# Kernel tuning notes

Measured on AMD Instinct MI355X. Metric: run time of the kernel, lower is better.

The kernel has to match this reference:

```python
import jax, jax.numpy as jnp
import numpy as np

W_PRIOR_STD = 1.0          # w_prior_stddev
OBS_STD = 1.0              # observational_noise_stddev
EPS = 1e-7                 # keras backend.epsilon()
B, E, K, C = 64, 32, 128, 512


def setup_inputs() -> dict:
    key = jax.random.key(0)
    k1, k2, k3, k4 = jax.random.split(key, 4)
    x = jax.random.normal(k1, (B, E, C), jnp.float32)
    prior_memory_mean = jax.random.normal(k2, (K, C), jnp.float32)  # truncated_normal(0,1) init
    prior_log_variance_scale = jax.random.uniform(k3, (), jnp.float32)  # scalar weight (init zeros; nonzero for testing)
    log_w_stddev = jnp.float32(0.3)  # constant(initial_w_stddev) init
    z_noise = jax.random.normal(k4, (E, B, C), jnp.float32)  # reparam noise for z_distribution.sample()
    return {"x": x, "prior_memory_mean": prior_memory_mean,
            "prior_log_variance_scale": prior_log_variance_scale,
            "log_w_stddev": log_w_stddev, "z_noise": z_noise}


def _kl_w(w, sw, k):
    # KL( N(w, sw^2 I_k) || N(0, w_prior^2 I_k) ), w_prior = 1
    return 0.5 * (k * sw * sw + jnp.sum(w * w, axis=-1) - k - 2.0 * k * jnp.log(sw))


def reference(x, prior_memory_mean, prior_log_variance_scale, log_w_stddev, z_noise):
    b, e, c = x.shape
    k = prior_memory_mean.shape[0]
    dt = x.dtype
    sw = jnp.exp(log_w_stddev)                      # w_stddev
    lam = (OBS_STD ** 2) / (W_PRIOR_STD ** 2)       # l2 regularizer in w-solve
    I_k = jnp.eye(k, dtype=dt)

    # prior state (tiled over batch)
    M0 = jnp.broadcast_to(prior_memory_mean[None], (b, k, c)) + jnp.zeros((b, k, c), dt)
    var = prior_log_variance_scale + EPS
    U0 = jnp.broadcast_to(var * I_k, (b, k, k)) + jnp.zeros((b, k, k), dt)

    z = jnp.transpose(x, (1, 0, 2))  # [E,B,C]

    def solve_w(M, z_t):
        # least squares: w = (M M^T + lam I)^{-1} M z  -> [B,K]
        A = jnp.einsum('bkc,blc->bkl', M, M) + lam * I_k
        rhs = jnp.einsum('bkc,bc->bk', M, z_t)
        return jnp.linalg.solve(A, rhs[..., None])[..., 0]

    def step(carry, z_t):
        M, U = carry                                    # [B,K,C], [B,K,K]
        w = solve_w(M, z_t)                             # memory sample == mean; iteration_count == 1
        delta = z_t - jnp.einsum('bk,bkc->bc', w, M)    # prediction delta [B,C]
        wU = jnp.einsum('bk,bkl->bl', w, U)             # cross variance [B,K]
        sigma = jnp.sum(wU * w, axis=-1) + OBS_STD ** 2 # z episode covariance [B]
        gain = wU / sigma[:, None]                      # [B,K]
        M_new = M + gain[..., None] * delta[:, None, :] # rank-1 Kalman update
        U_new = U - jnp.einsum('bk,bl->bkl', gain, wU)
        return (M_new, U_new), _kl_w(w, sw, k)          # per-step w divergence [B]

    (M_post, U_post), kl_episode = jax.lax.scan(step, (M0, U0), z)  # kl_episode [E,B]

    # read memory: batched solve with shared Gram matrix over episode
    A = jnp.einsum('bkc,blc->bkl', M_post, M_post) + lam * I_k
    rhs = jnp.einsum('bkc,ebc->bke', M_post, z)
    w_read = jnp.transpose(jnp.linalg.solve(A, rhs), (2, 0, 1))     # [E,B,K]
    z_mean = jnp.einsum('ebk,bkc->ebc', w_read, M_post)
    kl_read = _kl_w(w_read, sw, k)                                  # [E,B]

    total_divergence = jnp.mean(kl_episode + kl_read)               # add_loss value
    z_sample = z_mean + OBS_STD * z_noise                           # reparameterized sample
    return jnp.transpose(z_sample, (1, 0, 2)), total_divergence
```

## Files before the change

### kernel.cpp

```cpp
#include <hip/hip_runtime.h>

#define BB 64
#define EE 32
#define KK 128
#define CC 512
#define V0EPS 1e-7f

#define LTR 132
#define PTS 132
#define LKM 36
#define L36 36
#define LWT 176
#define SEG(i) ((((i) >> 4) * 20) + ((i) & 15))

#define SC_S2  0
#define SC_SIG 1
#define SC_KL  2
#define SC_B1  3
#define SC_B2  4
#define SC_R11 5
#define SC_R12 6
#define SC_R22 7

__device__ __forceinline__ float wsum64(float v) {
#pragma unroll
  for (int m = 32; m >= 1; m >>= 1) v += __shfl_xor(v, m, 64);
  return v;
}

__device__ __forceinline__ float wsum32(float v) {
#pragma unroll
  for (int m = 16; m >= 1; m >>= 1) v += __shfl_xor(v, m, 64);
  return v;
}

__device__ __forceinline__ float dot4(const float4 a, const float4 b) {
  return a.x * b.x + a.y * b.y + a.z * b.z + a.w * b.w;
}

__global__ __launch_bounds__(256) void a0_kernel(const float* __restrict__ M0,
                                                 float* __restrict__ wsA0) {
  __shared__ __align__(16) float sRow[CC];
  const int k = blockIdx.x >> 1, half = blockIdx.x & 1;
  for (int c = threadIdx.x; c < CC; c += 256) sRow[c] = M0[k * CC + c];
  __syncthreads();
  const int wv = threadIdx.x >> 6, ln = threadIdx.x & 63;
  const float4* zr = (const float4*)(sRow + 8 * ln);
  const float4 z0 = zr[0], z1 = zr[1];
  for (int li = 0; li < 16; ++li) {
    const int l = half * 64 + wv * 16 + li;
    const float4* rp = (const float4*)(M0 + l * CC + 8 * ln);
    const float4 a = rp[0], b = rp[1];
    float s = dot4(a, z0) + dot4(b, z1);
    s = wsum64(s);
    if (ln == 0) wsA0[k * KK + l] = s + (l == k ? 1.0f : 0.0f);
  }
}

__global__ __launch_bounds__(1024) void psinv_kernel(const float* __restrict__ x,
                                                     const float* __restrict__ M0,
                                                     float* __restrict__ wsP,
                                                     float* __restrict__ wsSp,
                                                     const float* __restrict__ A0g,
                                                     float* __restrict__ Ainv0) {
  __shared__ __align__(16) float zAll[32][520];
  __shared__ __align__(16) float Mch[2][16][520];
  __shared__ float sFb[2][128];
  __shared__ __align__(16) float sPv[2][256];
  __shared__ float sScal[2];
  const int tid = threadIdx.x;

  if (blockIdx.x > 0) {
    const int b = (blockIdx.x - 1) >> 2, kq = (blockIdx.x - 1) & 3;
    {
      const float4* x4 = (const float4*)(x + (size_t)b * EE * CC);
#pragma unroll
      for (int i = 0; i < 4; i++) {
        const int F = tid + 1024 * i, e = F >> 7, c4 = F & 127;
        ((float4*)zAll[e])[c4] = x4[F];
      }
    }
    const float4* M4 = (const float4*)M0;
    const int srow = tid >> 7, sc4 = tid & 127;
    const int kbase = kq * 32;
    float4 st0 = M4[(kbase + srow) * 128 + sc4];
    float4 st1 = M4[(kbase + 8 + srow) * 128 + sc4];
    int buf = 0;
    const int p = tid & 7;
    const int ep = (tid >> 3) & 15;
    const int kp = tid >> 7;
#pragma unroll 1
    for (int kc = 0; kc < 2; ++kc) {
      ((float4*)Mch[buf][srow])[sc4] = st0;
      ((float4*)Mch[buf][8 + srow])[sc4] = st1;
      __syncthreads();
      if (kc == 0) {
        st0 = M4[(kbase + 16 + srow) * 128 + sc4];
        st1 = M4[(kbase + 24 + srow) * 128 + sc4];
      }
      float s00 = 0, s01 = 0, s10 = 0, s11 = 0;
      const float* m0 = Mch[buf][kp];
      const float* m1 = Mch[buf][kp + 8];
      const float* z0 = zAll[2 * ep];
      const float* z1 = zAll[2 * ep + 1];
#pragma unroll
      for (int u = 0; u < 16; u++) {
        const int c = 4 * p + 32 * u;
        const float4 a0 = *(const float4*)(m0 + c);
        const float4 a1 = *(const float4*)(m1 + c);
        const float4 b0 = *(const float4*)(z0 + c);
        const float4 b1 = *(const float4*)(z1 + c);
        s00 += dot4(a0, b0); s01 += dot4(a0, b1);
        s10 += dot4(a1, b0); s11 += dot4(a1, b1);
      }
#pragma unroll
      for (int m = 1; m <= 4; m <<= 1) {
        s00 += __shfl_xor(s00, m, 64); s01 += __shfl_xor(s01, m, 64);
        s10 += __shfl_xor(s10, m, 64); s11 += __shfl_xor(s11, m, 64);
      }
      if (p == 0) {
        float* Pb = wsP + (size_t)b * KK * EE;
        Pb[(kbase + kc * 16 + kp) * EE + 2 * ep] = s00;
        Pb[(kbase + kc * 16 + kp) * EE + 2 * ep + 1] = s01;
        Pb[(kbase + kc * 16 + kp + 8) * EE + 2 * ep] = s10;
        Pb[(kbase + kc * 16 + kp + 8) * EE + 2 * ep + 1] = s11;
      }
      buf ^= 1;
    }
    {
      const int e = tid >> 5, f = tid & 31;
      const float4* ze = ((const float4*)zAll[e]) + 32 * kq;
      const float4* zf = ((const float4*)zAll[f]) + 32 * kq;
      float a0 = 0, a1 = 0, a2 = 0, a3 = 0;
#pragma unroll 4
      for (int u = 0; u < 32; u++) {
        const float4 A = ze[u], Bq = zf[u];
        a0 += A.x * Bq.x; a1 += A.y * Bq.y; a2 += A.z * Bq.z; a3 += A.w * Bq.w;
      }
      wsSp[((size_t)b * 4 + kq) * 1024 + e * EE + f] = (a0 + a1) + (a2 + a3);
    }
  } else {
    const int r = tid >> 3, q = tid & 7;
    float wreg[16], vreg[16];
    {
      const float4* a4 = (const float4*)(A0g + r * KK + 16 * q);
#pragma unroll
      for (int u = 0; u < 4; u++) {
        const float4 t4 = a4[u];
        wreg[4 * u] = t4.x; wreg[4 * u + 1] = t4.y; wreg[4 * u + 2] = t4.z; wreg[4 * u + 3] = t4.w;
      }
#pragma unroll
      for (int c = 0; c < 16; c++) vreg[c] = (16 * q + c == r) ? 1.0f : 0.0f;
    }
    if (q == 0) sFb[0][r] = wreg[0];
    if (r == 0) {
#pragma unroll
      for (int c = 0; c < 16; c++) { sPv[0][16 * q + c] = wreg[c]; sPv[0][128 + 16 * q + c] = vreg[c]; }
    }
    if (tid == 0) sScal[0] = 1.0f / wreg[0];
    __syncthreads();
#pragma unroll 1
    for (int j = 0; j < KK; ++j) {
      const int sl = j & 1, sn = sl ^ 1;
      const float f = sFb[sl][r] * sScal[sl];
      if (r != j) {
        if (16 * q + 15 >= j) {
          const float4* w4 = (const float4*)(sPv[sl] + 16 * q);
#pragma unroll
          for (int u = 0; u < 4; u++) {
            const float4 aa = w4[u];
            wreg[4 * u] -= f * aa.x; wreg[4 * u + 1] -= f * aa.y;
            wreg[4 * u + 2] -= f * aa.z; wreg[4 * u + 3] -= f * aa.w;
          }
        }
        if (16 * q <= j) {
          const float4* v4 = (const float4*)(sPv[sl] + 128 + 16 * q);
#pragma unroll
          for (int u = 0; u < 4; u++) {
            const float4 bb = v4[u];
            vreg[4 * u] -= f * bb.x; vreg[4 * u + 1] -= f * bb.y;
            vreg[4 * u + 2] -= f * bb.z; vreg[4 * u + 3] -= f * bb.w;
          }
        }
      }
      if (j + 1 < KK) {
        const int jn = j + 1;
        float wval = 0.0f;
#pragma unroll
        for (int c = 0; c < 16; c++) if (c == (jn & 15)) wval = wreg[c];
        if (q == (jn >> 4)) sFb[sn][r] = wval;
        if (r == jn) {
#pragma unroll
          for (int c = 0; c < 16; c++) { sPv[sn][16 * q + c] = wreg[c]; sPv[sn][128 + 16 * q + c] = vreg[c]; }
        }
        if (r == jn && q == (jn >> 4)) sScal[sn] = 1.0f / wval;
      }
      __syncthreads();
    }
    {
      float dval = 0.0f;
#pragma unroll
      for (int c = 0; c < 16; c++) if (c == (r & 15)) dval = wreg[c];
      if (q == (r >> 4)) sFb[0][r] = dval;
    }
    __syncthreads();
    {
      const float sc = 1.0f / sFb[0][r];
      float4* o4 = (float4*)(Ainv0 + r * KK + 16 * q);
#pragma unroll
      for (int u = 0; u < 4; u++) {
        float4 o;
        o.x = vreg[4 * u] * sc; o.y = vreg[4 * u + 1] * sc;
        o.z = vreg[4 * u + 2] * sc; o.w = vreg[4 * u + 3] * sc;
        o4[u] = o;
      }
    }
  }
}

__global__ __launch_bounds__(1024) void scan_kernel(
    const float* __restrict__ Pg, const float* __restrict__ Sg,
    const float* __restrict__ scaleP, const float* __restrict__ Ainv0,
    float* __restrict__ wsKL, float* __restrict__ wsKLr, float* __restrict__ wsWt) {
  __shared__ __align__(16) float sPT[EE * PTS];
  __shared__ __align__(16) float sGT[EE * LTR];
  __shared__ __align__(16) float sEggT[EE * LTR];
  __shared__ __align__(16) float uni2[EE * LTR];
  __shared__ __align__(16) float uni3[KK * LKM];
  __shared__ __align__(16) float uni1[KK * LKM];
  __shared__ __align__(16) float sEk[KK * LKM];
  __shared__ __align__(16) float sS[EE * L36];
  __shared__ __align__(16) float sD[EE * L36];
  __shared__ __align__(16) float sW[160];
  __shared__ __align__(16) float sWU[160];
  __shared__ __align__(16) float sPu[160];
  __shared__ __align__(16) float sPm[160];
  __shared__ __align__(16) float sQ[160];
  __shared__ __align__(16) float sDz[EE];
  __shared__ __align__(16) float sDgw[EE];
  __shared__ __align__(16) float sQt[EE];
  __shared__ __align__(16) float sScal[16];

  float* sYT = uni2;
  float* sGk = uni3;
  float* sYk = uni1;

  const int tid = threadIdx.x, ln = tid & 63;
  const int mr = (tid >> 2) & 127, mq = tid & 3;
  const int b = blockIdx.x;

  float areg[32];
  if (tid < 512) {
    const float4* a4 = (const float4*)(Ainv0 + mr * KK + 32 * mq);
#pragma unroll
    for (int u = 0; u < 8; u++) {
      const float4 t4 = a4[u];
      areg[4 * u] = t4.x; areg[4 * u + 1] = t4.y; areg[4 * u + 2] = t4.z; areg[4 * u + 3] = t4.w;
    }
  }
  {
    const float* Pb = Pg + (size_t)b * KK * EE;
#pragma unroll
    for (int i = 0; i < 4; i++) {
      const int idx = tid + 1024 * i;
      sPT[(idx & 31) * PTS + (idx >> 5)] = Pb[idx];
    }
    const float* Sb = Sg + (size_t)b * 4096;
    sS[(tid >> 5) * L36 + (tid & 31)] =
        Sb[tid] + Sb[tid + 1024] + Sb[tid + 2048] + Sb[tid + 3072];
  }
  if (tid < 16) sScal[tid] = 0.0f;
  const float v0 = scaleP[0] + V0EPS;
  __syncthreads();
  if (tid < 512) {
    const float* xb = sPT + 32 * mq;
    float s = 0;
#pragma unroll
    for (int c = 0; c < 32; c++) s += areg[c] * xb[c];
    s += __shfl_xor(s, 1, 64); s += __shfl_xor(s, 2, 64);
    if (mq == 0) sW[SEG(mr)] = s;
  }
  __syncthreads();

#pragma unroll 1
  for (int t = 0; t < EE; ++t) {
    const bool hn = (t + 1 < EE);
    if (tid < 512) {
      const float* xb = sW + 40 * mq;
      float s = 0;
#pragma unroll
      for (int c = 0; c < 16; c++) s += areg[c] * xb[c];
#pragma unroll
      for (int c = 0; c < 16; c++) s += areg[16 + c] * xb[20 + c];
      s += __shfl_xor(s, 1, 64); s += __shfl_xor(s, 2, 64);
      if (mq == 0) sPm[SEG(mr)] = s;
    } else if (tid < 768) {
      const int s8 = (tid - 512) >> 3, p3 = tid & 7;
      if (s8 < t) {
        const float* gr = sGT + s8 * LTR + 16 * p3;
        const float* wr_ = sW + 20 * p3;
        float s = 0;
#pragma unroll
        for (int kk = 0; kk < 16; kk++) s += gr[kk] * wr_[kk];
        s += __shfl_xor(s, 1, 64); s += __shfl_xor(s, 2, 64); s += __shfl_xor(s, 4, 64);
        if (p3 == 0) sDgw[s8] = s;
      } else if (s8 == 31) {
        const float* wp = sW + 20 * p3;
        float s = 0;
#pragma unroll
        for (int kk = 0; kk < 16; kk++) s += wp[kk] * wp[kk];
        s += __shfl_xor(s, 1, 64); s += __shfl_xor(s, 2, 64); s += __shfl_xor(s, 4, 64);
        if (p3 == 0) sScal[SC_S2] = s;
      }
    } else {
      const int j = (tid - 768) >> 3, p3 = tid & 7;
      if (j < t) {
        const float* yr = sYT + j * LTR + 16 * p3;
        const float* wr_ = sW + 20 * p3;
        float s = 0;
#pragma unroll
        for (int kk = 0; kk < 16; kk++) s += yr[kk] * wr_[kk];
        s += __shfl_xor(s, 1, 64); s += __shfl_xor(s, 2, 64); s += __shfl_xor(s, 4, 64);
        if (p3 == 0) sQt[j] = s;
      }
    }
    __syncthreads();
    if (tid < 256) {
      const int k = tid >> 1, h = tid & 1;
      const float* yk = sYk + k * LKM + 16 * h;
      const float* qb = sQt + 16 * h;
      float a = 0;
#pragma unroll
      for (int u = 0; u < 16; u++) {
        const int j = 16 * h + u;
        a += (j < t) ? yk[u] * qb[u] : 0.0f;
      }
      a += __shfl_xor(a, 1, 64);
      if (h == 0) sWU[SEG(k)] = v0 * sW[SEG(k)] - a;
    } else if (tid < 384) {
      const int r2 = (tid - 256) >> 2, p = tid & 3;
      float a = 0;
#pragma unroll
      for (int u = 0; u < 8; u++) {
        const int s2 = p + 4 * u;
        a += (s2 < t) ? sDgw[s2] * sD[s2 * L36 + r2] : 0.0f;
      }
      a += __shfl_xor(a, 1, 64); a += __shfl_xor(a, 2, 64);
      if (p == 0) sD[t * L36 + r2] = ((r2 == t) ? 1.0f : 0.0f) - a;
    } else if (tid < 448) {
      float a = sW[SEG(ln)] * sPm[SEG(ln)] + sW[SEG(ln + 64)] * sPm[SEG(ln + 64)];
      a = wsum64(a);
      if (ln == 0) sScal[SC_R22] = a;
    } else if (tid < 512) {
      const float s2v = sScal[SC_S2];
      float a = (ln < t) ? sQt[ln] * sQt[ln] : 0.0f;
      a = wsum64(a);
      if (ln == 0) {
        sScal[SC_SIG] = v0 * s2v - a + 1.0f;
        sScal[SC_KL] += s2v;
      }
    } else if (tid < 640) {
      const int k = tid - 512;
      float a = sW[SEG(k)];
      const float* ek = sEk + k * LKM;
      const int nc = (t + 3) >> 2;
#pragma unroll 1
      for (int c4 = 0; c4 < nc; ++c4) {
        const float4 ev = *(const float4*)(ek + 4 * c4);
        const float4 dv = *(const float4*)(sDgw + 4 * c4);
        const int u0 = 4 * c4;
        a -= ((u0 + 0 < t) ? ev.x * dv.x : 0.0f) + ((u0 + 1 < t) ? ev.y * dv.y : 0.0f) +
             ((u0 + 2 < t) ? ev.z * dv.z : 0.0f) + ((u0 + 3 < t) ? ev.w * dv.w : 0.0f);
      }
      sEk[k * LKM + t] = a;
      sEggT[t * LTR + k] = a;
    } else if (tid < 896) {
      const int s4 = (tid - 640) >> 3, p3 = tid & 7;
      if (hn && s4 < t) {
        const float* er = sEggT + s4 * LTR + 16 * p3;
        const float* pr = sPT + (t + 1) * PTS + 16 * p3;
        float a = 0;
#pragma unroll
        for (int kk = 0; kk < 16; kk++) a -= er[kk] * pr[kk];
        const float4 dv = *(const float4*)(sD + s4 * L36 + 4 * p3);
        const float4 sv = *(const float4*)(sS + (t + 1) * L36 + 4 * p3);
        a += dot4(dv, sv);
        a += __shfl_xor(a, 1, 64); a += __shfl_xor(a, 2, 64); a += __shfl_xor(a, 4, 64);
        if (p3 == 0) sDz[s4] = a;
      }
    }
    __syncthreads();
    if (tid < 512) {
      const float* xb = sWU + 40 * mq;
      float s = 0;
#pragma unroll
      for (int c = 0; c < 16; c++) s += areg[c] * xb[c];
#pragma unroll
      for (int c = 0; c < 16; c++) s += areg[16 + c] * xb[20 + c];
      s += __shfl_xor(s, 1, 64); s += __shfl_xor(s, 2, 64);
      if (mq == 0) sPu[SEG(mr)] = s;
    } else if (tid < 576) {
      if (hn) {
        float a = -(sEggT[t * LTR + ln] * sPT[(t + 1) * PTS + ln] +
                    sEggT[t * LTR + ln + 64] * sPT[(t + 1) * PTS + ln + 64]);
        if (ln < 32) a += sD[t * L36 + ln] * sS[(t + 1) * L36 + ln];
        a = wsum64(a);
        if (ln == 0) sDz[t] = a;
      }
    } else if (tid < 640) {
      float a = sEggT[t * LTR + ln] * sPT[t * PTS + ln] +
                sEggT[t * LTR + ln + 64] * sPT[t * PTS + ln + 64];
      a = wsum64(a);
      if (ln == 0) sScal[SC_B2] = a;
    } else if (tid < 704) {
      if (ln < 32) {
        float a = sD[t * L36 + ln] * sS[t * L36 + ln];
        a = wsum32(a);
        if (ln == 0) sScal[SC_B1] = a;
      } else {
        const int k0 = (ln - 32) * 4;
        const float4 wu4 = *(const float4*)(sWU + SEG(k0));
        const float4 pm4 = *(const float4*)(sPm + SEG(k0));
        float a = dot4(wu4, pm4);
        a = wsum32(a);
        if (ln == 32) sScal[SC_R12] = a;
      }
    } else if (tid < 768) {
      const float sig = sScal[SC_SIG];
      const float rsq = rsqrtf(sig);
#pragma unroll
      for (int u = 0; u < 2; u++) {
        const int k = ln + 64 * u;
        const float wu = sWU[SEG(k)];
        const float gv = wu / sig;
        const float yv = wu * rsq;
        sGT[t * LTR + k] = gv;
        sGk[k * LKM + t] = gv;
        sYT[t * LTR + k] = yv;
        sYk[k * LKM + t] = yv;
      }
    }
    __syncthreads();
    if (tid < 512) {
      if (hn) {
        const float* gk = sGk + mr * LKM + 8 * mq;
        const float* dzb = sDz + 8 * mq;
        float a = 0;
#pragma unroll
        for (int u = 0; u < 8; u++) {
          const int s2 = 8 * mq + u;
          a += (s2 < t) ? gk[u] * dzb[u] : 0.0f;
        }
        a += __shfl_xor(a, 1, 64); a += __shfl_xor(a, 2, 64);
        if (mq == 0)
          sQ[SEG(mr)] = sPT[(t + 1) * PTS + mr] + a + (sWU[SEG(mr)] / sScal[SC_SIG]) * sDz[t];
      }
    } else if (tid < 576) {
      float a = sWU[SEG(ln)] * sPu[SEG(ln)] + sWU[SEG(ln + 64)] * sPu[SEG(ln + 64)];
      a = wsum64(a);
      if (ln == 0) sScal[SC_R11] = a;
    }
    __syncthreads();
    if (tid < 512) {
      {
        const float4 sc0 = *(const float4*)(sScal);
        const float4 sc1 = *(const float4*)(sScal + 4);
        const float rs = 1.0f / sc0.y;
        const float beta = sc0.w - sc1.x - sc0.x;
        const float e11 = sc1.y * rs * rs;
        const float e12 = sc1.z * rs + 1.0f;
        const float e22 = sc1.w - beta;
        const float rd = 1.0f / (e11 * e22 - e12 * e12);
        const float t11 = e22 * rd, t12 = -e12 * rd, t22 = e11 * rd;
        const float u1r = sPu[SEG(mr)] * rs, u2r = sPm[SEG(mr)];
        const float* pub = sPu + 40 * mq;
        const float* pmb = sPm + 40 * mq;
#pragma unroll
        for (int c = 0; c < 16; c++) {
          const float u1c = pub[c] * rs;
          const float u2c = pmb[c];
          areg[c] -= u1r * (t11 * u1c + t12 * u2c) + u2r * (t12 * u1c + t22 * u2c);
        }
#pragma unroll
        for (int c = 0; c < 16; c++) {
          const float u1c = pub[20 + c] * rs;
          const float u2c = pmb[20 + c];
          areg[16 + c] -= u1r * (t11 * u1c + t12 * u2c) + u2r * (t12 * u1c + t22 * u2c);
        }
      }
      if (hn) {
        const float* xb = sQ + 40 * mq;
        float s = 0;
#pragma unroll
        for (int c = 0; c < 16; c++) s += areg[c] * xb[c];
#pragma unroll
        for (int c = 0; c < 16; c++) s += areg[16 + c] * xb[20 + c];
        s += __shfl_xor(s, 1, 64); s += __shfl_xor(s, 2, 64);
        if (mq == 0) sW[SEG(mr)] = s;
      }
    }
    __syncthreads();
  }

  float* sR1T  = uni2;
  float* sGamT = uni2 + 1152;
  float* sRhsT = uni1;
  float* sWrT  = uni3;
  if (tid == 0) wsKL[b] = sScal[SC_KL];

  {
    const int s = tid >> 5, e = tid & 31;
    const float4* er = (const float4*)(sEggT + s * LTR);
    const float4* pr = (const float4*)(sPT + e * PTS);
    float a = 0;
#pragma unroll 8
    for (int u = 0; u < 32; ++u) a -= dot4(er[u], pr[u]);
    const float4* dr = (const float4*)(sD + s * L36);
    const float4* sr = (const float4*)(sS + e * L36);
#pragma unroll
    for (int u = 0; u < 8; ++u) a += dot4(dr[u], sr[u]);
    sR1T[e * 36 + s] = a;
  }
  __syncthreads();
  {
    const int k = tid & 127, e8 = tid >> 7;
    float4 g0, g1, g2, g3, g4, g5, g6, g7;
    {
      const float4* gk = (const float4*)(sGk + k * LKM);
      g0 = gk[0]; g1 = gk[1]; g2 = gk[2]; g3 = gk[3];
      g4 = gk[4]; g5 = gk[5]; g6 = gk[6]; g7 = gk[7];
    }
#pragma unroll
    for (int u = 0; u < 4; ++u) {
      const int e = e8 * 4 + u;
      const float4* r1 = (const float4*)(sR1T + e * 36);
      float a = sPT[e * PTS + k];
      a += dot4(g0, r1[0]) + dot4(g1, r1[1]) + dot4(g2, r1[2]) + dot4(g3, r1[3]);
      a += dot4(g4, r1[4]) + dot4(g5, r1[5]) + dot4(g6, r1[6]) + dot4(g7, r1[7]);
      sRhsT[e * PTS + k] = a;
    }
  }
  __syncthreads();
  if (tid < 512) {
#pragma unroll 2
    for (int e = 0; e < EE; ++e) {
      const float* xb = sRhsT + e * PTS + 32 * mq;
      float s = 0;
#pragma unroll
      for (int c = 0; c < 32; c++) s += areg[c] * xb[c];
      s += __shfl_xor(s, 1, 64); s += __shfl_xor(s, 2, 64);
      if (mq == 0) sWrT[e * PTS + mr] = s;
    }
  }
  __syncthreads();
  {
    const int s = tid >> 5, e = tid & 31;
    const float4* gr = (const float4*)(sGT + s * LTR);
    const float4* wr = (const float4*)(sWrT + e * PTS);
    float a = 0;
#pragma unroll 8
    for (int u = 0; u < 32; ++u) a += dot4(gr[u], wr[u]);
    sGamT[e * 36 + s] = a;
  }
  __syncthreads();
  {
    const int k = tid & 127, e8 = tid >> 7;
    float4 E0, E1, E2, E3, E4, E5, E6, E7;
    {
      const float4* ek = (const float4*)(sEk + k * LKM);
      E0 = ek[0]; E1 = ek[1]; E2 = ek[2]; E3 = ek[3];
      E4 = ek[4]; E5 = ek[5]; E6 = ek[6]; E7 = ek[7];
    }
#pragma unroll
    for (int u = 0; u < 4; ++u) {
      const int e = e8 * 4 + u;
      const float4* gm = (const float4*)(sGamT + e * 36);
      float a = sWrT[e * PTS + k];
      a -= dot4(E0, gm[0]) + dot4(E1, gm[1]) + dot4(E2, gm[2]) + dot4(E3, gm[3]);
      a -= dot4(E4, gm[4]) + dot4(E5, gm[5]) + dot4(E6, gm[6]) + dot4(E7, gm[7]);
      wsWt[(size_t)b * 5120 + e * 160 + k] = a;
    }
  }
  {
    const int e = tid & 31, sp = tid >> 5;
    float4 gm[8];
    {
      const float4* g4 = (const float4*)(sGamT + e * 36);
#pragma unroll
      for (int u = 0; u < 8; ++u) gm[u] = g4[u];
    }
    float a = 0;
#pragma unroll
    for (int u = 0; u < 8; ++u) {
      const float4 g = gm[u];
      a += sD[(4 * u + 0) * L36 + sp] * g.x + sD[(4 * u + 1) * L36 + sp] * g.y +
           sD[(4 * u + 2) * L36 + sp] * g.z + sD[(4 * u + 3) * L36 + sp] * g.w;
    }
    wsWt[(size_t)b * 5120 + e * 160 + 128 + sp] = a;
  }
  {
    const int e = tid >> 5, p = tid & 31;
    const float4 w0 = *(const float4*)(sWrT + e * PTS + 4 * p);
    float a = dot4(w0, w0);
    a = wsum32(a);
    if ((tid & 31) == 0) wsKLr[b * EE + e] = a;
  }
}

__global__ __launch_bounds__(512) void postBF_kernel(
    const float* __restrict__ wsWt, const float* __restrict__ x,
    const float* __restrict__ M0, const float* __restrict__ znoise,
    const float* __restrict__ wsKL, const float* __restrict__ wsKLr,
    const float* __restrict__ lwsP, float* __restrict__ out) {
  __shared__ __align__(16) float sWtT[32 * LWT];
  __shared__ __align__(16) float Mch[2 * 16 * 132];
  const int tid = threadIdx.x;

  if (blockIdx.x == 256) {
    float* sPp = sWtT;
    float s = 0.0f;
    if (tid < 64) s += wsKL[tid];
    for (int i = tid; i < 2048; i += 512) s += wsKLr[i];
    sPp[tid] = s;
    __syncthreads();
    for (int off = 256; off > 0; off >>= 1) {
      if (tid < off) sPp[tid] += sPp[tid + off];
      __syncthreads();
    }
    if (tid == 0) {
      const float lws = lwsP[0];
      const float sw2 = expf(2.0f * lws);
      out[(size_t)BB * EE * CC] =
          0.5f * sPp[0] / (float)(EE * BB) + (float)KK * (sw2 - 1.0f - 2.0f * lws);
    }
    return;
  }

  const int b = blockIdx.x >> 2, cq = blockIdx.x & 3;
  {
    const int e = tid >> 4, j = tid & 15;
    const float* Wg = wsWt + (size_t)b * 5120 + e * 160;
#pragma unroll
    for (int u = 0; u < 10; ++u) sWtT[e * LWT + j + 16 * u] = Wg[j + 16 * u];
  }
  const int srow = tid >> 5, sc4 = tid & 31;
  const int e = tid & 31, cs = tid >> 5;
  const float* xb = x + (size_t)b * EE * CC;
  const int cbase = cq * 128;
  float4 st = *(const float4*)(M0 + srow * CC + cbase + 4 * sc4);
  float acc[8];
#pragma unroll
  for (int u = 0; u < 8; u++) acc[u] = 0.0f;
  int buf = 0;
#pragma unroll 1
  for (int ch2 = 0; ch2 < 10; ++ch2) {
    *(float4*)(Mch + buf * 2112 + srow * 132 + 4 * sc4) = st;
    __syncthreads();
    if (ch2 + 1 < 10) {
      const int row = (ch2 + 1) * 16 + srow;
      st = (row < 128) ? *(const float4*)(M0 + row * CC + cbase + 4 * sc4)
                       : *(const float4*)(xb + (row - 128) * CC + cbase + 4 * sc4);
    }
    const float4* wt4 = (const float4*)(sWtT + e * LWT + ch2 * 16);
    const float4 wa = wt4[0], wb = wt4[1], wc = wt4[2], wd = wt4[3];
    const float wv16[16] = {wa.x, wa.y, wa.z, wa.w, wb.x, wb.y, wb.z, wb.w,
                            wc.x, wc.y, wc.z, wc.w, wd.x, wd.y, wd.z, wd.w};
#pragma unroll
    for (int kk = 0; kk < 16; ++kk) {
      const float* mrp = Mch + buf * 2112 + kk * 132 + cs * 8;
      const float4 m0 = *(const float4*)(mrp);
      const float4 m1 = *(const float4*)(mrp + 4);
      const float wk = wv16[kk];
      acc[0] += wk * m0.x; acc[1] += wk * m0.y; acc[2] += wk * m0.z; acc[3] += wk * m0.w;
      acc[4] += wk * m1.x; acc[5] += wk * m1.y; acc[6] += wk * m1.z; acc[7] += wk * m1.w;
    }
    buf ^= 1;
  }
  {
    const size_t ob = ((size_t)b * EE + e) * CC + cbase + cs * 8;
    const size_t nb = ((size_t)e * BB + b) * CC + cbase + cs * 8;
#pragma unroll
    for (int u = 0; u < 2; u++) {
      const float4 nz = *(const float4*)(znoise + nb + 4 * u);
      float4 o;
      o.x = acc[4 * u] + nz.x;     o.y = acc[4 * u + 1] + nz.y;
      o.z = acc[4 * u + 2] + nz.z; o.w = acc[4 * u + 3] + nz.w;
      *(float4*)(out + ob + 4 * u) = o;
    }
  }
}

extern "C" void kernel_launch(void* const* d_in, const int* in_sizes, int n_in,
                              void* d_out, int out_size, void* d_ws, size_t ws_size,
                              hipStream_t stream) {
  (void)in_sizes; (void)n_in; (void)out_size; (void)ws_size;
  const float* x = (const float*)d_in[0];
  const float* M0 = (const float*)d_in[1];
  const float* scaleP = (const float*)d_in[2];
  const float* lwsP = (const float*)d_in[3];
  const float* znoise = (const float*)d_in[4];
  float* out = (float*)d_out;

  float* ws = (float*)d_ws;
  float* wsP = ws;
  float* wsSp = wsP + 262144;
  float* wsA0 = wsSp + 262144;
  float* wsAinv0 = wsA0 + 16384;
  float* wsKL = wsAinv0 + 16384;
  float* wsKLr = wsKL + 64;
  float* wsWt = wsKLr + 2048;

  a0_kernel<<<256, 256, 0, stream>>>(M0, wsA0);
  psinv_kernel<<<257, 1024, 0, stream>>>(x, M0, wsP, wsSp, wsA0, wsAinv0);
  scan_kernel<<<BB, 1024, 0, stream>>>(wsP, wsSp, scaleP, wsAinv0,
                                       wsKL, wsKLr, wsWt);
  postBF_kernel<<<257, 512, 0, stream>>>(wsWt, x, M0, znoise, wsKL, wsKLr, lwsP, out);
}
```

Before: 287.9 us.

## Block Gauss-Jordan inversion two pivots per step to halve barriers

The Gauss-Jordan inverse of the initial Gram matrix in block 0 of psinv_kernel now eliminates two pivot columns per iteration using a 2x2 block pivot. This runs 64 iterations and 64 barriers instead of 128, with double-buffered shared pivot rows and columns. The cost is more shared loads and arithmetic per iteration and a slightly different rounding order. It only helps if block 0's serial inversion is on the critical path relative to the other blocks.

```diff
diff --git a/kernel.cpp b/kernel.cpp
--- a/kernel.cpp
+++ b/kernel.cpp
@@ -65,9 +65,8 @@
                                                      float* __restrict__ Ainv0) {
   __shared__ __align__(16) float zAll[32][520];
   __shared__ __align__(16) float Mch[2][16][520];
-  __shared__ float sFb[2][128];
-  __shared__ __align__(16) float sPv[2][256];
-  __shared__ float sScal[2];
+  __shared__ __align__(16) float sFb[2][2][128];
+  __shared__ __align__(16) float sPv[2][2][256];
   const int tid = threadIdx.x;
 
   if (blockIdx.x > 0) {
@@ -152,48 +151,72 @@
 #pragma unroll
       for (int c = 0; c < 16; c++) vreg[c] = (16 * q + c == r) ? 1.0f : 0.0f;
     }
-    if (q == 0) sFb[0][r] = wreg[0];
+    if (q == 0) { sFb[0][0][r] = wreg[0]; sFb[0][1][r] = wreg[1]; }
     if (r == 0) {
 #pragma unroll
-      for (int c = 0; c < 16; c++) { sPv[0][16 * q + c] = wreg[c]; sPv[0][128 + 16 * q + c] = vreg[c]; }
-    }
-    if (tid == 0) sScal[0] = 1.0f / wreg[0];
+      for (int c = 0; c < 16; c++) { sPv[0][0][16 * q + c] = wreg[c]; sPv[0][0][128 + 16 * q + c] = vreg[c]; }
+    }
+    if (r == 1) {
+#pragma unroll
+      for (int c = 0; c < 16; c++) { sPv[0][1][16 * q + c] = wreg[c]; sPv[0][1][128 + 16 * q + c] = vreg[c]; }
+    }
     __syncthreads();
 #pragma unroll 1
-    for (int j = 0; j < KK; ++j) {
-      const int sl = j & 1, sn = sl ^ 1;
-      const float f = sFb[sl][r] * sScal[sl];
-      if (r != j) {
-        if (16 * q + 15 >= j) {
-          const float4* w4 = (const float4*)(sPv[sl] + 16 * q);
-#pragma unroll
-          for (int u = 0; u < 4; u++) {
-            const float4 aa = w4[u];
-            wreg[4 * u] -= f * aa.x; wreg[4 * u + 1] -= f * aa.y;
-            wreg[4 * u + 2] -= f * aa.z; wreg[4 * u + 3] -= f * aa.w;
-          }
+    for (int jj = 0; jj < 64; ++jj) {
+      const int j = 2 * jj, db = jj & 1, dn = db ^ 1;
+      const float* c0 = sFb[db][0];
+      const float* c1 = sFb[db][1];
+      const float* rj = sPv[db][0];
+      const float* rj1 = sPv[db][1];
+      const float p00 = c0[j], p10 = c0[j + 1], p01 = c1[j], p11 = c1[j + 1];
+      const float rp00 = 1.0f / p00;
+      const float g = p10 * rp00;
+      const float rp11 = 1.0f / (p11 - g * p01);
+      const float alpha = (r == j) ? 0.0f : c0[r] * rp00;
+      const float beta = (r == j + 1) ? 0.0f : (c1[r] - alpha * p01) * rp11;
+      const float ca = alpha - beta * g, cb = beta;
+      if (16 * q + 15 >= j) {
+        const float4* w0 = (const float4*)(rj + 16 * q);
+        const float4* w1 = (const float4*)(rj1 + 16 * q);
+#pragma unroll
+        for (int u = 0; u < 4; u++) {
+          const float4 a0 = w0[u], a1 = w1[u];
+          wreg[4 * u]     -= ca * a0.x + cb * a1.x;
+          wreg[4 * u + 1] -= ca * a0.y + cb * a1.y;
+          wreg[4 * u + 2] -= ca * a0.z + cb * a1.z;
+          wreg[4 * u + 3] -= ca * a0.w + cb * a1.w;
         }
-        if (16 * q <= j) {
-          const float4* v4 = (const float4*)(sPv[sl] + 128 + 16 * q);
-#pragma unroll
-          for (int u = 0; u < 4; u++) {
-            const float4 bb = v4[u];
-            vreg[4 * u] -= f * bb.x; vreg[4 * u + 1] -= f * bb.y;
-            vreg[4 * u + 2] -= f * bb.z; vreg[4 * u + 3] -= f * bb.w;
-          }
+      }
+      if (16 * q <= j + 1) {
+        const float4* v0 = (const float4*)(rj + 128 + 16 * q);
+        const float4* v1 = (const float4*)(rj1 + 128 + 16 * q);
+#pragma unroll
+        for (int u = 0; u < 4; u++) {
+          const float4 a0 = v0[u], a1 = v1[u];
+          vreg[4 * u]     -= ca * a0.x + cb * a1.x;
+          vreg[4 * u + 1] -= ca * a0.y + cb * a1.y;
+          vreg[4 * u + 2] -= ca * a0.z + cb * a1.z;
+          vreg[4 * u + 3] -= ca * a0.w + cb * a1.w;
         }
       }
-      if (j + 1 < KK) {
-        const int jn = j + 1;
-        float wval = 0.0f;
-#pragma unroll
-        for (int c = 0; c < 16; c++) if (c == (jn & 15)) wval = wreg[c];
-        if (q == (jn >> 4)) sFb[sn][r] = wval;
-        if (r == jn) {
-#pragma unroll
-          for (int c = 0; c < 16; c++) { sPv[sn][16 * q + c] = wreg[c]; sPv[sn][128 + 16 * q + c] = vreg[c]; }
+      if (jj + 1 < 64) {
+        const int j2 = j + 2, j3 = j + 3;
+        float w2 = 0.0f, w3 = 0.0f;
+#pragma unroll
+        for (int c = 0; c < 16; c++) {
+          if (c == (j2 & 15)) w2 = wreg[c];
+          if (c == (j3 & 15)) w3 = wreg[c];
         }
-        if (r == jn && q == (jn >> 4)) sScal[sn] = 1.0f / wval;
+        if (q == (j2 >> 4)) sFb[dn][0][r] = w2;
+        if (q == (j3 >> 4)) sFb[dn][1][r] = w3;
+        if (r == j2) {
+#pragma unroll
+          for (int c = 0; c < 16; c++) { sPv[dn][0][16 * q + c] = wreg[c]; sPv[dn][0][128 + 16 * q + c] = vreg[c]; }
+        }
+        if (r == j3) {
+#pragma unroll
+          for (int c = 0; c < 16; c++) { sPv[dn][1][16 * q + c] = wreg[c]; sPv[dn][1][128 + 16 * q + c] = vreg[c]; }
+        }
       }
       __syncthreads();
     }
@@ -201,11 +224,11 @@
       float dval = 0.0f;
 #pragma unroll
       for (int c = 0; c < 16; c++) if (c == (r & 15)) dval = wreg[c];
-      if (q == (r >> 4)) sFb[0][r] = dval;
+      if (q == (r >> 4)) sFb[0][0][r] = dval;
     }
     __syncthreads();
     {
-      const float sc = 1.0f / sFb[0][r];
+      const float sc = 1.0f / sFb[0][0][r];
       float4* o4 = (float4*)(Ainv0 + r * KK + 16 * q);
 #pragma unroll
       for (int u = 0; u < 4; u++) {
```

New measurement: 270.9 us. -5.9%, faster.
